# Kernel tuning notes

Hardware: AMD Instinct MI355X
Metric: run time of the kernel (lower is better)

## Reference

```python
import jax, jax.numpy as jnp
import numpy as np

N = 50000      # nodes
K = 12         # neighbors per node (regular graph, required by e.view(-1, numNgbrs))
E = N * K      # edges, sorted by row
F_IN = 128
F_OUT = 128
ALPHA = 0.2    # LeakyReLU negative slope


def setup_inputs() -> dict:
    key = jax.random.key(0)
    k_x, k_col, k_ws, k_wn, k_a, k_b = jax.random.split(key, 6)
    x = jax.random.normal(k_x, (N, F_IN), dtype=jnp.float32)
    # edges sorted by destination row, exactly K per node
    row = jnp.repeat(jnp.arange(N, dtype=jnp.int32), K)
    col = jax.random.randint(k_col, (E,), 0, N, dtype=jnp.int32)
    adj_vals = jnp.ones((E,), dtype=jnp.float32)  # sparse adj values
    stdv = 1.0 / np.sqrt(F_OUT)
    W_self = jax.random.uniform(k_ws, (F_IN, F_OUT), jnp.float32, -stdv, stdv)
    W_neighbor = jax.random.uniform(k_wn, (F_IN, F_OUT), jnp.float32, -stdv, stdv)
    lim = 1.414 * np.sqrt(6.0 / (2 * F_OUT + 1))  # xavier_uniform gain=1.414 on [2F,1]
    a = jax.random.uniform(k_a, (2 * F_OUT,), jnp.float32, -lim, lim)
    bias = jax.random.uniform(k_b, (F_OUT,), jnp.float32, -stdv, stdv)
    return {"x": x, "adj_vals": adj_vals, "row": row, "col": col,
            "W_self": W_self, "W_neighbor": W_neighbor, "a": a, "bias": bias}


def reference(x, adj_vals, row, col, W_self, W_neighbor, a, bias):
    act_self = x @ W_self                       # [N, F_OUT]
    h = x @ W_neighbor                          # [N, F_OUT]
    # cat([h_in, h_out], 1) @ a  ==  h_in @ a[:F] + h_out @ a[F:]
    # precompute per-node dots, then gather per edge (cheaper than ExF gathers)
    s_in = h @ a[:F_OUT]                        # [N]
    s_out = h @ a[F_OUT:]                       # [N]
    e = jax.nn.leaky_relu(s_in[row] + s_out[col], ALPHA)   # [E]
    # per-destination-node softmax over its K contiguous edges
    att = jax.nn.softmax(e.reshape(N, K), axis=1).reshape(-1)  # [E]
    # attention-weighted sparse scatter-add aggregation
    msg = (adj_vals * att)[:, None] * h[col]    # [E, F_OUT]
    act_neighbor = jax.ops.segment_sum(msg, row, num_segments=N)
    return act_self + act_neighbor + bias
```

## Files before the change

### kernel.cpp

```cpp
#include <hip/hip_runtime.h>

constexpr int N_NODES = 50000;
constexpr int KNB = 12;
constexpr int F = 128;
constexpr float ALPHA = 0.2f;
constexpr int BM = 64;

typedef __bf16 bf16x8 __attribute__((ext_vector_type(8)));
typedef float  f32x4  __attribute__((ext_vector_type(4)));

__device__ __forceinline__ unsigned bfr(float f) {
    unsigned u = __float_as_uint(f);
    return (u + 0x7fffu + ((u >> 16) & 1u)) >> 16;
}
__device__ __forceinline__ unsigned pack2(float lo, float hi) {
    return bfr(lo) | (bfr(hi) << 16);
}
__device__ __forceinline__ float bf2f(unsigned bits16) {
    return __uint_as_float(bits16 << 16);
}

__global__ __launch_bounds__(256) void gat_prep(const float* __restrict__ Wself,
                                                const float* __restrict__ Wnb,
                                                unsigned* __restrict__ Wt) {
    const int gid = blockIdx.x * 256 + threadIdx.x;
    const int n  = gid >> 6;
    const int kp = gid & 63;
    const float* src = (n < F) ? (Wself + n) : (Wnb + (n - F));
    const float f0 = src[(size_t)(kp * 2)     * F];
    const float f1 = src[(size_t)(kp * 2 + 1) * F];
    Wt[n * 64 + kp] = pack2(f0, f1);
}

__global__ __launch_bounds__(256, 2) void gat_gemm(
    const float* __restrict__ x,
    const unsigned* __restrict__ Wt,
    const float* __restrict__ a,
    const float* __restrict__ bias,
    float* __restrict__ out,
    unsigned short* __restrict__ hb,
    float* __restrict__ s_in,
    float* __restrict__ s_out)
{
    __shared__ uint4 ldsX[BM * 16];
    __shared__ uint4 ldsW[256 * 16];

    const int t = threadIdx.x;
    const int base = blockIdx.x * BM;

#pragma unroll
    for (int i = 0; i < 4; ++i) {
        const int idx = t + i * 256;
        const int row = idx >> 4;
        const int k16 = idx & 15;
        int gr = base + row; if (gr >= N_NODES) gr = N_NODES - 1;
        const float4* xp = reinterpret_cast<const float4*>(x + (size_t)gr * F + k16 * 8);
        const float4 f0 = xp[0];
        const float4 f1 = xp[1];
        uint4 v;
        v.x = pack2(f0.x, f0.y); v.y = pack2(f0.z, f0.w);
        v.z = pack2(f1.x, f1.y); v.w = pack2(f1.z, f1.w);
        ldsX[row * 16 + (k16 ^ (row & 7))] = v;
    }
    const uint4* Wt4 = reinterpret_cast<const uint4*>(Wt);
#pragma unroll
    for (int i = 0; i < 16; ++i) {
        const int idx = t + i * 256;
        const int n   = idx >> 4;
        const int k16 = idx & 15;
        ldsW[n * 16 + (k16 ^ (n & 7))] = Wt4[idx];
    }
    __syncthreads();

    const int wid = t >> 6;
    const int lane = t & 63;
    const int lq = lane >> 4;
    const int lr = lane & 15;
    const int wm = wid >> 1;
    const int wn = wid & 1;

    const bf16x8* fx = reinterpret_cast<const bf16x8*>(ldsX);
    const bf16x8* fw = reinterpret_cast<const bf16x8*>(ldsW);

    f32x4 acc[2][8];
#pragma unroll
    for (int mt = 0; mt < 2; ++mt)
#pragma unroll
        for (int nt = 0; nt < 8; ++nt)
            acc[mt][nt] = f32x4{0.f, 0.f, 0.f, 0.f};

#pragma unroll
    for (int s = 0; s < 4; ++s) {
        bf16x8 af[2];
#pragma unroll
        for (int mt = 0; mt < 2; ++mt) {
            const int row = wm * 32 + mt * 16 + lr;
            af[mt] = fx[row * 16 + ((s * 4 + lq) ^ (row & 7))];
        }
        bf16x8 bw[8];
#pragma unroll
        for (int nt = 0; nt < 8; ++nt) {
            const int n = wn * 128 + nt * 16 + lr;
            bw[nt] = fw[n * 16 + ((s * 4 + lq) ^ (n & 7))];
        }
#pragma unroll
        for (int mt = 0; mt < 2; ++mt)
#pragma unroll
            for (int nt = 0; nt < 8; ++nt)
                acc[mt][nt] = __builtin_amdgcn_mfma_f32_16x16x32_bf16(af[mt], bw[nt], acc[mt][nt], 0, 0, 0);
    }

    if (wn == 0) {
        float bv[8];
#pragma unroll
        for (int nt = 0; nt < 8; ++nt) bv[nt] = bias[nt * 16 + lr];
#pragma unroll
        for (int mt = 0; mt < 2; ++mt)
#pragma unroll
            for (int r = 0; r < 4; ++r) {
                const int row = base + wm * 32 + mt * 16 + lq * 4 + r;
                if (row < N_NODES) {
#pragma unroll
                    for (int nt = 0; nt < 8; ++nt)
                        out[(size_t)row * F + nt * 16 + lr] = acc[mt][nt][r] + bv[nt];
                }
            }
    } else {
        float alo[8], ahi[8];
#pragma unroll
        for (int nt = 0; nt < 8; ++nt) {
            alo[nt] = a[nt * 16 + lr];
            ahi[nt] = a[F + nt * 16 + lr];
        }
#pragma unroll
        for (int mt = 0; mt < 2; ++mt)
#pragma unroll
            for (int r = 0; r < 4; ++r) {
                const int row = base + wm * 32 + mt * 16 + lq * 4 + r;
                float pin = 0.f, pout = 0.f;
#pragma unroll
                for (int nt = 0; nt < 8; ++nt) {
                    const float v = acc[mt][nt][r];
                    pin  = fmaf(v, alo[nt], pin);
                    pout = fmaf(v, ahi[nt], pout);
                }
#pragma unroll
                for (int msk = 8; msk >= 1; msk >>= 1) {
                    pin  += __shfl_xor(pin,  msk);
                    pout += __shfl_xor(pout, msk);
                }
                if (row < N_NODES) {
#pragma unroll
                    for (int nt = 0; nt < 8; ++nt)
                        hb[(size_t)row * F + nt * 16 + lr] = (unsigned short)bfr(acc[mt][nt][r]);
                    if (lr == 0) { s_in[row] = pin; s_out[row] = pout; }
                }
            }
    }
}

__global__ __launch_bounds__(256) void gat_attn(
    const unsigned* __restrict__ hb32,
    const float* __restrict__ s_in,
    const float* __restrict__ s_out,
    const int* __restrict__ colidx,
    const float* __restrict__ adj,
    float* __restrict__ out)
{
    const int wid = threadIdx.x >> 6;
    const int lane = threadIdx.x & 63;
    const int node = blockIdx.x * 4 + wid;

    float e = -1e30f;
    int c = 0;
    float av = 0.f;
    if (lane < KNB) {
        c  = colidx[node * KNB + lane];
        av = adj[node * KNB + lane];
        const float ev = s_in[node] + s_out[c];
        e = ev > 0.f ? ev : ALPHA * ev;
    }
    float m = e;
#pragma unroll
    for (int msk = 8; msk >= 1; msk >>= 1) m = fmaxf(m, __shfl_xor(m, msk));
    const float p = (lane < KNB) ? __expf(e - m) : 0.f;
    float ssum = p;
#pragma unroll
    for (int msk = 8; msk >= 1; msk >>= 1) ssum += __shfl_xor(ssum, msk);
    const float att = p / ssum * av;

    float accx = 0.f, accy = 0.f;
#pragma unroll
    for (int j = 0; j < KNB; ++j) {
        const float aj = __shfl(att, j);
        const int   cj = __shfl(c, j);
        const unsigned u = hb32[(size_t)cj * 64 + lane];
        accx = fmaf(aj, bf2f(u & 0xffffu), accx);
        accy = fmaf(aj, bf2f(u >> 16), accy);
    }
    float2* op = reinterpret_cast<float2*>(out + (size_t)node * F) + lane;
    float2 o = *op;
    o.x += accx; o.y += accy;
    *op = o;
}

extern "C" void kernel_launch(void* const* d_in, const int* in_sizes, int n_in,
                              void* d_out, int out_size, void* d_ws, size_t ws_size,
                              hipStream_t stream) {
    const float* x     = (const float*)d_in[0];
    const float* adj   = (const float*)d_in[1];
    const int*   col   = (const int*)d_in[3];
    const float* Wself = (const float*)d_in[4];
    const float* Wnb   = (const float*)d_in[5];
    const float* a     = (const float*)d_in[6];
    const float* bias  = (const float*)d_in[7];
    float* out = (float*)d_out;

    char* ws = (char*)d_ws;
    unsigned short* hb = (unsigned short*)ws;
    float* s_in  = (float*)(ws + 12800000);
    float* s_out = (float*)(ws + 13000000);
    unsigned* Wt = (unsigned*)(ws + 13200000);

    gat_prep<<<64, 256, 0, stream>>>(Wself, Wnb, Wt);
    gat_gemm<<<(N_NODES + BM - 1) / BM, 256, 0, stream>>>(x, Wt, a, bias, out, hb, s_in, s_out);
    gat_attn<<<N_NODES / 4, 256, 0, stream>>>((const unsigned*)hb, s_in, s_out, col, adj, out);
}
```

Baseline: 55.67 us.

## Fuse GEMM and attention aggregation into one kernel with a grid-wide barrier

Merges the projection GEMM and the attention/aggregation kernels into a single launch. Blocks grow to 256 rows and 512 threads, and each wave now computes both the self and neighbor projections. An atomic-counter spin barrier makes all blocks finish writing hb, s_in and s_out before any block gathers neighbors. This removes one launch and the write-then-read-modify-write of the output: the self term and bias stay in registers and are added to the aggregated messages at the final store. The cost is correctness that depends on all 196 blocks being co-resident, far fewer blocks than before for latency hiding, and a gather rewritten from 4-byte per-lane loads into 2-byte strided loads per 16-lane group.

```diff
diff --git a/kernel.cpp b/kernel.cpp
--- a/kernel.cpp
+++ b/kernel.cpp
@@ -4,7 +4,8 @@
 constexpr int KNB = 12;
 constexpr int F = 128;
 constexpr float ALPHA = 0.2f;
-constexpr int BM = 64;
+constexpr int BM = 256;
+constexpr int NBLK = (N_NODES + BM - 1) / BM;
 
 typedef __bf16 bf16x8 __attribute__((ext_vector_type(8)));
 typedef float  f32x4  __attribute__((ext_vector_type(4)));
@@ -32,15 +33,18 @@
     Wt[n * 64 + kp] = pack2(f0, f1);
 }
 
-__global__ __launch_bounds__(256, 2) void gat_gemm(
+__global__ __launch_bounds__(512, 2) void gat_fused(
     const float* __restrict__ x,
     const unsigned* __restrict__ Wt,
     const float* __restrict__ a,
     const float* __restrict__ bias,
+    const int* __restrict__ colidx,
+    const float* __restrict__ adj,
     float* __restrict__ out,
     unsigned short* __restrict__ hb,
     float* __restrict__ s_in,
-    float* __restrict__ s_out)
+    float* __restrict__ s_out,
+    unsigned* __restrict__ cnt)
 {
     __shared__ uint4 ldsX[BM * 16];
     __shared__ uint4 ldsW[256 * 16];
@@ -48,9 +52,17 @@
     const int t = threadIdx.x;
     const int base = blockIdx.x * BM;
 
-#pragma unroll
-    for (int i = 0; i < 4; ++i) {
-        const int idx = t + i * 256;
+    const uint4* Wt4 = reinterpret_cast<const uint4*>(Wt);
+#pragma unroll
+    for (int i = 0; i < 8; ++i) {
+        const int idx = t + i * 512;
+        const int n   = idx >> 4;
+        const int k16 = idx & 15;
+        ldsW[n * 16 + (k16 ^ (n & 7))] = Wt4[idx];
+    }
+#pragma unroll
+    for (int i = 0; i < 8; ++i) {
+        const int idx = t + i * 512;
         const int row = idx >> 4;
         const int k16 = idx & 15;
         int gr = base + row; if (gr >= N_NODES) gr = N_NODES - 1;
@@ -62,31 +74,21 @@
         v.z = pack2(f1.x, f1.y); v.w = pack2(f1.z, f1.w);
         ldsX[row * 16 + (k16 ^ (row & 7))] = v;
     }
-    const uint4* Wt4 = reinterpret_cast<const uint4*>(Wt);
-#pragma unroll
-    for (int i = 0; i < 16; ++i) {
-        const int idx = t + i * 256;
-        const int n   = idx >> 4;
-        const int k16 = idx & 15;
-        ldsW[n * 16 + (k16 ^ (n & 7))] = Wt4[idx];
-    }
     __syncthreads();
 
-    const int wid = t >> 6;
+    const int w    = t >> 6;
     const int lane = t & 63;
-    const int lq = lane >> 4;
-    const int lr = lane & 15;
-    const int wm = wid >> 1;
-    const int wn = wid & 1;
+    const int lq   = lane >> 4;
+    const int lr   = lane & 15;
 
     const bf16x8* fx = reinterpret_cast<const bf16x8*>(ldsX);
     const bf16x8* fw = reinterpret_cast<const bf16x8*>(ldsW);
 
-    f32x4 acc[2][8];
+    f32x4 acc[2][16];
 #pragma unroll
     for (int mt = 0; mt < 2; ++mt)
 #pragma unroll
-        for (int nt = 0; nt < 8; ++nt)
+        for (int nt = 0; nt < 16; ++nt)
             acc[mt][nt] = f32x4{0.f, 0.f, 0.f, 0.f};
 
 #pragma unroll
@@ -94,114 +96,111 @@
         bf16x8 af[2];
 #pragma unroll
         for (int mt = 0; mt < 2; ++mt) {
-            const int row = wm * 32 + mt * 16 + lr;
+            const int row = w * 32 + mt * 16 + lr;
             af[mt] = fx[row * 16 + ((s * 4 + lq) ^ (row & 7))];
         }
-        bf16x8 bw[8];
-#pragma unroll
-        for (int nt = 0; nt < 8; ++nt) {
-            const int n = wn * 128 + nt * 16 + lr;
-            bw[nt] = fw[n * 16 + ((s * 4 + lq) ^ (n & 7))];
-        }
-#pragma unroll
-        for (int mt = 0; mt < 2; ++mt)
-#pragma unroll
-            for (int nt = 0; nt < 8; ++nt)
-                acc[mt][nt] = __builtin_amdgcn_mfma_f32_16x16x32_bf16(af[mt], bw[nt], acc[mt][nt], 0, 0, 0);
-    }
-
-    if (wn == 0) {
-        float bv[8];
-#pragma unroll
-        for (int nt = 0; nt < 8; ++nt) bv[nt] = bias[nt * 16 + lr];
-#pragma unroll
-        for (int mt = 0; mt < 2; ++mt)
-#pragma unroll
-            for (int r = 0; r < 4; ++r) {
-                const int row = base + wm * 32 + mt * 16 + lq * 4 + r;
-                if (row < N_NODES) {
-#pragma unroll
-                    for (int nt = 0; nt < 8; ++nt)
-                        out[(size_t)row * F + nt * 16 + lr] = acc[mt][nt][r] + bv[nt];
+#pragma unroll
+        for (int half = 0; half < 2; ++half) {
+            bf16x8 bw[8];
+#pragma unroll
+            for (int j = 0; j < 8; ++j) {
+                const int n = half * 128 + j * 16 + lr;
+                bw[j] = fw[n * 16 + ((s * 4 + lq) ^ (n & 7))];
+            }
+#pragma unroll
+            for (int mt = 0; mt < 2; ++mt)
+#pragma unroll
+                for (int j = 0; j < 8; ++j)
+                    acc[mt][half * 8 + j] =
+                        __builtin_amdgcn_mfma_f32_16x16x32_bf16(af[mt], bw[j], acc[mt][half * 8 + j], 0, 0, 0);
+        }
+    }
+
+    float alo[8], ahi[8], bias_v[8];
+#pragma unroll
+    for (int j = 0; j < 8; ++j) {
+        alo[j]    = a[j * 16 + lr];
+        ahi[j]    = a[F + j * 16 + lr];
+        bias_v[j] = bias[j * 16 + lr];
+    }
+#pragma unroll
+    for (int mt = 0; mt < 2; ++mt)
+#pragma unroll
+        for (int r = 0; r < 4; ++r) {
+            const int row = base + w * 32 + mt * 16 + lq * 4 + r;
+            float pin = 0.f, pout = 0.f;
+#pragma unroll
+            for (int j = 0; j < 8; ++j) {
+                const float v = acc[mt][8 + j][r];
+                pin  = fmaf(v, alo[j], pin);
+                pout = fmaf(v, ahi[j], pout);
+            }
+#pragma unroll
+            for (int msk = 8; msk >= 1; msk >>= 1) {
+                pin  += __shfl_xor(pin,  msk);
+                pout += __shfl_xor(pout, msk);
+            }
+            if (row < N_NODES) {
+#pragma unroll
+                for (int j = 0; j < 8; ++j)
+                    hb[(size_t)row * F + j * 16 + lr] = (unsigned short)bfr(acc[mt][8 + j][r]);
+                if (lr == 0) { s_in[row] = pin; s_out[row] = pout; }
+            }
+        }
+
+    __threadfence();
+    __syncthreads();
+    if (t == 0) {
+        atomicAdd(cnt, 1u);
+        while (atomicAdd(cnt, 0u) < (unsigned)NBLK) __builtin_amdgcn_s_sleep(8);
+    }
+    __syncthreads();
+    __threadfence();
+
+#pragma unroll
+    for (int mt = 0; mt < 2; ++mt)
+#pragma unroll
+        for (int r = 0; r < 4; ++r) {
+            const int row = base + w * 32 + mt * 16 + lq * 4 + r;
+            const bool valid = (row < N_NODES);
+            int   c  = 0;
+            float av = 0.f;
+            float e  = -1e30f;
+            if (valid && lr < KNB) {
+                c  = colidx[row * KNB + lr];
+                av = adj[row * KNB + lr];
+                const float ev = s_in[row] + s_out[c];
+                e = ev > 0.f ? ev : ALPHA * ev;
+            }
+            float m = e;
+#pragma unroll
+            for (int msk = 8; msk >= 1; msk >>= 1) m = fmaxf(m, __shfl_xor(m, msk));
+            const float p = (lr < KNB) ? __expf(e - m) : 0.f;
+            float ssum = p;
+#pragma unroll
+            for (int msk = 8; msk >= 1; msk >>= 1) ssum += __shfl_xor(ssum, msk);
+            const float att = p / ssum * av;
+
+            float agg[8];
+#pragma unroll
+            for (int j = 0; j < 8; ++j) agg[j] = 0.f;
+            const int gbase = lane & 48;
+#pragma unroll
+            for (int j = 0; j < KNB; ++j) {
+                const float aj = __shfl(att, gbase + j);
+                const int   cj = __shfl(c,   gbase + j);
+                const unsigned short* hp = hb + (size_t)cj * F + lr;
+#pragma unroll
+                for (int nt = 0; nt < 8; ++nt) {
+                    agg[nt] = fmaf(aj, bf2f((unsigned)hp[nt * 16]), agg[nt]);
                 }
             }
-    } else {
-        float alo[8], ahi[8];
-#pragma unroll
-        for (int nt = 0; nt < 8; ++nt) {
-            alo[nt] = a[nt * 16 + lr];
-            ahi[nt] = a[F + nt * 16 + lr];
-        }
-#pragma unroll
-        for (int mt = 0; mt < 2; ++mt)
-#pragma unroll
-            for (int r = 0; r < 4; ++r) {
-                const int row = base + wm * 32 + mt * 16 + lq * 4 + r;
-                float pin = 0.f, pout = 0.f;
-#pragma unroll
-                for (int nt = 0; nt < 8; ++nt) {
-                    const float v = acc[mt][nt][r];
-                    pin  = fmaf(v, alo[nt], pin);
-                    pout = fmaf(v, ahi[nt], pout);
-                }
-#pragma unroll
-                for (int msk = 8; msk >= 1; msk >>= 1) {
-                    pin  += __shfl_xor(pin,  msk);
-                    pout += __shfl_xor(pout, msk);
-                }
-                if (row < N_NODES) {
-#pragma unroll
-                    for (int nt = 0; nt < 8; ++nt)
-                        hb[(size_t)row * F + nt * 16 + lr] = (unsigned short)bfr(acc[mt][nt][r]);
-                    if (lr == 0) { s_in[row] = pin; s_out[row] = pout; }
-                }
-            }
-    }
-}
-
-__global__ __launch_bounds__(256) void gat_attn(
-    const unsigned* __restrict__ hb32,
-    const float* __restrict__ s_in,
-    const float* __restrict__ s_out,
-    const int* __restrict__ colidx,
-    const float* __restrict__ adj,
-    float* __restrict__ out)
-{
-    const int wid = threadIdx.x >> 6;
-    const int lane = threadIdx.x & 63;
-    const int node = blockIdx.x * 4 + wid;
-
-    float e = -1e30f;
-    int c = 0;
-    float av = 0.f;
-    if (lane < KNB) {
-        c  = colidx[node * KNB + lane];
-        av = adj[node * KNB + lane];
-        const float ev = s_in[node] + s_out[c];
-        e = ev > 0.f ? ev : ALPHA * ev;
-    }
-    float m = e;
-#pragma unroll
-    for (int msk = 8; msk >= 1; msk >>= 1) m = fmaxf(m, __shfl_xor(m, msk));
-    const float p = (lane < KNB) ? __expf(e - m) : 0.f;
-    float ssum = p;
-#pragma unroll
-    for (int msk = 8; msk >= 1; msk >>= 1) ssum += __shfl_xor(ssum, msk);
-    const float att = p / ssum * av;
-
-    float accx = 0.f, accy = 0.f;
-#pragma unroll
-    for (int j = 0; j < KNB; ++j) {
-        const float aj = __shfl(att, j);
-        const int   cj = __shfl(c, j);
-        const unsigned u = hb32[(size_t)cj * 64 + lane];
-        accx = fmaf(aj, bf2f(u & 0xffffu), accx);
-        accy = fmaf(aj, bf2f(u >> 16), accy);
-    }
-    float2* op = reinterpret_cast<float2*>(out + (size_t)node * F) + lane;
-    float2 o = *op;
-    o.x += accx; o.y += accy;
-    *op = o;
+            if (valid) {
+#pragma unroll
+                for (int nt = 0; nt < 8; ++nt)
+                    out[(size_t)row * F + nt * 16 + lr] = acc[mt][nt][r] + bias_v[nt] + agg[nt];
+            }
+        }
 }
 
 extern "C" void kernel_launch(void* const* d_in, const int* in_sizes, int n_in,
@@ -221,8 +220,9 @@
     float* s_in  = (float*)(ws + 12800000);
     float* s_out = (float*)(ws + 13000000);
     unsigned* Wt = (unsigned*)(ws + 13200000);
-
+    unsigned* cnt = (unsigned*)(ws + 13266944);
+
+    hipMemsetAsync(cnt, 0, 4, stream);
     gat_prep<<<64, 256, 0, stream>>>(Wself, Wnb, Wt);
-    gat_gemm<<<(N_NODES + BM - 1) / BM, 256, 0, stream>>>(x, Wt, a, bias, out, hb, s_in, s_out);
-    gat_attn<<<N_NODES / 4, 256, 0, stream>>>((const unsigned*)hb, s_in, s_out, col, adj, out);
-}
+    gat_fused<<<NBLK, 512, 0, stream>>>(x, Wt, a, bias, col, adj, out, hb, s_in, s_out, cnt);
+}
```

Result: slower. 144.8 us (+160.1%).

## Transpose GEMM tiling for vectorized epilogue stores and split attention gather across half-waves

Applied to the files above, without the earlier changes.

The GEMM now computes W^T·X^T so each lane holds four contiguous output columns. This allows float4 stores to out and packed uint2 bf16 stores to h, where the old code did scalar stores. The attention dot products are reduced through shared memory across the two h-waves, which adds two extra barriers. The attention kernel splits the 12 neighbors between the two half-waves using 8-byte gathers and then combines them with a cross-half shuffle, issuing fewer but wider loads.

```diff
diff --git a/kernel.cpp b/kernel.cpp
--- a/kernel.cpp
+++ b/kernel.cpp
@@ -48,6 +48,14 @@
     const int t = threadIdx.x;
     const int base = blockIdx.x * BM;
 
+    const uint4* Wt4 = reinterpret_cast<const uint4*>(Wt);
+#pragma unroll
+    for (int i = 0; i < 16; ++i) {
+        const int idx = t + i * 256;
+        const int n   = idx >> 4;
+        const int k16 = idx & 15;
+        ldsW[n * 16 + (k16 ^ (n & 7))] = Wt4[idx];
+    }
 #pragma unroll
     for (int i = 0; i < 4; ++i) {
         const int idx = t + i * 256;
@@ -62,114 +70,120 @@
         v.z = pack2(f1.x, f1.y); v.w = pack2(f1.z, f1.w);
         ldsX[row * 16 + (k16 ^ (row & 7))] = v;
     }
-    const uint4* Wt4 = reinterpret_cast<const uint4*>(Wt);
-#pragma unroll
-    for (int i = 0; i < 16; ++i) {
-        const int idx = t + i * 256;
-        const int n   = idx >> 4;
-        const int k16 = idx & 15;
-        ldsW[n * 16 + (k16 ^ (n & 7))] = Wt4[idx];
-    }
     __syncthreads();
 
-    const int wid = t >> 6;
+    const int w    = t >> 6;
     const int lane = t & 63;
-    const int lq = lane >> 4;
-    const int lr = lane & 15;
-    const int wm = wid >> 1;
-    const int wn = wid & 1;
+    const int lq   = lane >> 4;
+    const int lr   = lane & 15;
 
     const bf16x8* fx = reinterpret_cast<const bf16x8*>(ldsX);
     const bf16x8* fw = reinterpret_cast<const bf16x8*>(ldsW);
 
-    f32x4 acc[2][8];
-#pragma unroll
-    for (int mt = 0; mt < 2; ++mt)
-#pragma unroll
-        for (int nt = 0; nt < 8; ++nt)
-            acc[mt][nt] = f32x4{0.f, 0.f, 0.f, 0.f};
+    f32x4 acc[4][4];
+#pragma unroll
+    for (int mt = 0; mt < 4; ++mt)
+#pragma unroll
+        for (int rt = 0; rt < 4; ++rt)
+            acc[mt][rt] = f32x4{0.f, 0.f, 0.f, 0.f};
 
 #pragma unroll
     for (int s = 0; s < 4; ++s) {
-        bf16x8 af[2];
-#pragma unroll
-        for (int mt = 0; mt < 2; ++mt) {
-            const int row = wm * 32 + mt * 16 + lr;
-            af[mt] = fx[row * 16 + ((s * 4 + lq) ^ (row & 7))];
-        }
-        bf16x8 bw[8];
-#pragma unroll
-        for (int nt = 0; nt < 8; ++nt) {
-            const int n = wn * 128 + nt * 16 + lr;
-            bw[nt] = fw[n * 16 + ((s * 4 + lq) ^ (n & 7))];
-        }
-#pragma unroll
-        for (int mt = 0; mt < 2; ++mt)
-#pragma unroll
-            for (int nt = 0; nt < 8; ++nt)
-                acc[mt][nt] = __builtin_amdgcn_mfma_f32_16x16x32_bf16(af[mt], bw[nt], acc[mt][nt], 0, 0, 0);
-    }
-
-    if (wn == 0) {
-        float bv[8];
-#pragma unroll
-        for (int nt = 0; nt < 8; ++nt) bv[nt] = bias[nt * 16 + lr];
-#pragma unroll
-        for (int mt = 0; mt < 2; ++mt)
-#pragma unroll
-            for (int r = 0; r < 4; ++r) {
-                const int row = base + wm * 32 + mt * 16 + lq * 4 + r;
+        bf16x8 wf[4], xf[4];
+#pragma unroll
+        for (int mt = 0; mt < 4; ++mt) {
+            const int n = w * 64 + mt * 16 + lr;
+            wf[mt] = fw[n * 16 + ((s * 4 + lq) ^ (n & 7))];
+        }
+#pragma unroll
+        for (int rt = 0; rt < 4; ++rt) {
+            const int r = rt * 16 + lr;
+            xf[rt] = fx[r * 16 + ((s * 4 + lq) ^ (r & 7))];
+        }
+#pragma unroll
+        for (int mt = 0; mt < 4; ++mt)
+#pragma unroll
+            for (int rt = 0; rt < 4; ++rt)
+                acc[mt][rt] = __builtin_amdgcn_mfma_f32_16x16x32_bf16(wf[mt], xf[rt], acc[mt][rt], 0, 0, 0);
+    }
+
+    __syncthreads();
+    float* sbuf = reinterpret_cast<float*>(ldsX);
+
+    if (w < 2) {
+#pragma unroll
+        for (int mt = 0; mt < 4; ++mt) {
+            const int col0 = w * 64 + mt * 16 + lq * 4;
+            const float4 b4 = *reinterpret_cast<const float4*>(bias + col0);
+#pragma unroll
+            for (int rt = 0; rt < 4; ++rt) {
+                const int row = base + rt * 16 + lr;
                 if (row < N_NODES) {
-#pragma unroll
-                    for (int nt = 0; nt < 8; ++nt)
-                        out[(size_t)row * F + nt * 16 + lr] = acc[mt][nt][r] + bv[nt];
+                    const f32x4 v = acc[mt][rt];
+                    float4 o{v[0] + b4.x, v[1] + b4.y, v[2] + b4.z, v[3] + b4.w};
+                    *reinterpret_cast<float4*>(out + (size_t)row * F + col0) = o;
                 }
             }
+        }
     } else {
-        float alo[8], ahi[8];
-#pragma unroll
-        for (int nt = 0; nt < 8; ++nt) {
-            alo[nt] = a[nt * 16 + lr];
-            ahi[nt] = a[F + nt * 16 + lr];
-        }
-#pragma unroll
-        for (int mt = 0; mt < 2; ++mt)
-#pragma unroll
-            for (int r = 0; r < 4; ++r) {
-                const int row = base + wm * 32 + mt * 16 + lq * 4 + r;
-                float pin = 0.f, pout = 0.f;
-#pragma unroll
-                for (int nt = 0; nt < 8; ++nt) {
-                    const float v = acc[mt][nt][r];
-                    pin  = fmaf(v, alo[nt], pin);
-                    pout = fmaf(v, ahi[nt], pout);
+        float spin[4] = {0.f, 0.f, 0.f, 0.f};
+        float spout[4] = {0.f, 0.f, 0.f, 0.f};
+#pragma unroll
+        for (int mt = 0; mt < 4; ++mt) {
+            const int colh0 = (w - 2) * 64 + mt * 16 + lq * 4;
+            const float4 al = *reinterpret_cast<const float4*>(a + colh0);
+            const float4 ah = *reinterpret_cast<const float4*>(a + F + colh0);
+#pragma unroll
+            for (int rt = 0; rt < 4; ++rt) {
+                const int row = base + rt * 16 + lr;
+                const f32x4 v = acc[mt][rt];
+                if (row < N_NODES) {
+                    uint2 pk{pack2(v[0], v[1]), pack2(v[2], v[3])};
+                    *reinterpret_cast<uint2*>(hb + (size_t)row * F + colh0) = pk;
                 }
-#pragma unroll
-                for (int msk = 8; msk >= 1; msk >>= 1) {
-                    pin  += __shfl_xor(pin,  msk);
-                    pout += __shfl_xor(pout, msk);
-                }
-                if (row < N_NODES) {
-#pragma unroll
-                    for (int nt = 0; nt < 8; ++nt)
-                        hb[(size_t)row * F + nt * 16 + lr] = (unsigned short)bfr(acc[mt][nt][r]);
-                    if (lr == 0) { s_in[row] = pin; s_out[row] = pout; }
-                }
+                spin[rt]  = fmaf(v[0], al.x, fmaf(v[1], al.y, fmaf(v[2], al.z, fmaf(v[3], al.w, spin[rt]))));
+                spout[rt] = fmaf(v[0], ah.x, fmaf(v[1], ah.y, fmaf(v[2], ah.z, fmaf(v[3], ah.w, spout[rt]))));
             }
+        }
+#pragma unroll
+        for (int rt = 0; rt < 4; ++rt) {
+            spin[rt]  += __shfl_xor(spin[rt], 16);
+            spin[rt]  += __shfl_xor(spin[rt], 32);
+            spout[rt] += __shfl_xor(spout[rt], 16);
+            spout[rt] += __shfl_xor(spout[rt], 32);
+        }
+        if (lq == 0) {
+#pragma unroll
+            for (int rt = 0; rt < 4; ++rt) {
+                sbuf[(w - 2) * 128 + rt * 16 + lr]      = spin[rt];
+                sbuf[(w - 2) * 128 + 64 + rt * 16 + lr] = spout[rt];
+            }
+        }
+    }
+    __syncthreads();
+    if (t < 128) {
+        const int i = t & 63;
+        const int row = base + i;
+        if (row < N_NODES) {
+            if (t < 64) s_in[row]  = sbuf[i] + sbuf[128 + i];
+            else        s_out[row] = sbuf[64 + i] + sbuf[192 + i];
+        }
     }
 }
 
 __global__ __launch_bounds__(256) void gat_attn(
-    const unsigned* __restrict__ hb32,
+    const uint2* __restrict__ hbU2,
     const float* __restrict__ s_in,
     const float* __restrict__ s_out,
     const int* __restrict__ colidx,
     const float* __restrict__ adj,
     float* __restrict__ out)
 {
-    const int wid = threadIdx.x >> 6;
+    const int wid  = threadIdx.x >> 6;
     const int lane = threadIdx.x & 63;
     const int node = blockIdx.x * 4 + wid;
+    const int half = lane >> 5;
+    const int hl   = lane & 31;
 
     float e = -1e30f;
     int c = 0;
@@ -189,19 +203,29 @@
     for (int msk = 8; msk >= 1; msk >>= 1) ssum += __shfl_xor(ssum, msk);
     const float att = p / ssum * av;
 
-    float accx = 0.f, accy = 0.f;
-#pragma unroll
-    for (int j = 0; j < KNB; ++j) {
-        const float aj = __shfl(att, j);
-        const int   cj = __shfl(c, j);
-        const unsigned u = hb32[(size_t)cj * 64 + lane];
-        accx = fmaf(aj, bf2f(u & 0xffffu), accx);
-        accy = fmaf(aj, bf2f(u >> 16), accy);
-    }
-    float2* op = reinterpret_cast<float2*>(out + (size_t)node * F) + lane;
-    float2 o = *op;
-    o.x += accx; o.y += accy;
-    *op = o;
+    float4 acc{0.f, 0.f, 0.f, 0.f};
+    const int sbase = half * 6;
+#pragma unroll
+    for (int i = 0; i < 6; ++i) {
+        const float aj = __shfl(att, sbase + i);
+        const int   cj = __shfl(c,   sbase + i);
+        const uint2 u = hbU2[(size_t)cj * 32 + hl];
+        acc.x = fmaf(aj, bf2f(u.x & 0xffffu), acc.x);
+        acc.y = fmaf(aj, bf2f(u.x >> 16),     acc.y);
+        acc.z = fmaf(aj, bf2f(u.y & 0xffffu), acc.z);
+        acc.w = fmaf(aj, bf2f(u.y >> 16),     acc.w);
+    }
+    acc.x += __shfl_xor(acc.x, 32);
+    acc.y += __shfl_xor(acc.y, 32);
+    acc.z += __shfl_xor(acc.z, 32);
+    acc.w += __shfl_xor(acc.w, 32);
+
+    if (lane < 32) {
+        float4* op = reinterpret_cast<float4*>(out + (size_t)node * F) + hl;
+        float4 o = *op;
+        o.x += acc.x; o.y += acc.y; o.z += acc.z; o.w += acc.w;
+        *op = o;
+    }
 }
 
 extern "C" void kernel_launch(void* const* d_in, const int* in_sizes, int n_in,
@@ -224,5 +248,5 @@
 
     gat_prep<<<64, 256, 0, stream>>>(Wself, Wnb, Wt);
     gat_gemm<<<(N_NODES + BM - 1) / BM, 256, 0, stream>>>(x, Wt, a, bias, out, hb, s_in, s_out);
-    gat_attn<<<N_NODES / 4, 256, 0, stream>>>((const unsigned*)hb, s_in, s_out, col, adj, out);
-}
+    gat_attn<<<N_NODES / 4, 256, 0, stream>>>((const uint2*)hb, s_in, s_out, col, adj, out);
+}
```

After: 56.58 us. No clear change (+1.6%).
